# Optimization experiments

Hardware: AMD Instinct MI355X
Metric: run time of the kernel (lower is better)

Reference implementation:

```python
import jax, jax.numpy as jnp
from jax import lax
import numpy as np

GROUPS = 32  # EMA 'factor'
EPS = 1e-5   # torch GroupNorm default eps


def setup_inputs() -> dict:
    key = jax.random.key(0)
    ks = jax.random.split(key, 3)
    B, C, H, W = 8, 256, 128, 128
    cg = C // GROUPS  # channels per group = 8
    x = jax.random.normal(ks[0], (B, C, H, W), dtype=jnp.float32)
    w1 = jax.random.normal(ks[1], (cg, cg), dtype=jnp.float32) * 0.1    # conv1x1 weight (O,I)
    b1 = jnp.zeros((cg,), dtype=jnp.float32)
    w3 = jax.random.normal(ks[2], (cg, cg, 3, 3), dtype=jnp.float32) * 0.1  # conv3x3 weight (O,I,kh,kw)
    b3 = jnp.zeros((cg,), dtype=jnp.float32)
    gn_w = jnp.ones((cg,), dtype=jnp.float32)
    gn_b = jnp.zeros((cg,), dtype=jnp.float32)
    return {"x": x, "w1": w1, "b1": b1, "w3": w3, "b3": b3, "gn_w": gn_w, "gn_b": gn_b}


def reference(x, w1, b1, w3, b3, gn_w, gn_b):
    b, c, h, w = x.shape
    g = GROUPS
    cg = c // g
    gx = x.reshape(b * g, cg, h, w)                       # [bg, cg, h, w]
    # directional pooling (AdaptiveAvgPool over one axis)
    x_h = gx.mean(axis=3, keepdims=True)                  # [bg, cg, h, 1]
    x_w = gx.mean(axis=2, keepdims=True).transpose(0, 1, 3, 2)  # [bg, cg, w, 1]
    hw = jnp.concatenate([x_h, x_w], axis=2)              # [bg, cg, h+w, 1]
    hw = jnp.einsum('oi,bilk->bolk', w1, hw) + b1[None, :, None, None]
    xh = hw[:, :, :h]                                      # [bg, cg, h, 1]
    xw = hw[:, :, h:].transpose(0, 1, 3, 2)                # [bg, cg, 1, w]
    gated = gx * jax.nn.sigmoid(xh) * jax.nn.sigmoid(xw)
    # GroupNorm(cg groups over cg channels) == per-channel norm over (h, w)
    mu = gated.mean(axis=(2, 3), keepdims=True)
    var = gated.var(axis=(2, 3), keepdims=True)
    x1 = (gated - mu) / jnp.sqrt(var + EPS) * gn_w[None, :, None, None] + gn_b[None, :, None, None]
    # 3x3 conv branch
    x2 = lax.conv_general_dilated(gx, w3, (1, 1), 'SAME',
                                  dimension_numbers=('NCHW', 'OIHW', 'NCHW'))
    x2 = x2 + b3[None, :, None, None]
    # cross-branch channel-attention matmuls
    x11 = jax.nn.softmax(x1.mean(axis=(2, 3)), axis=-1)[:, None, :]  # [bg, 1, cg]
    x21 = jax.nn.softmax(x2.mean(axis=(2, 3)), axis=-1)[:, None, :]  # [bg, 1, cg]
    x12 = x2.reshape(b * g, cg, h * w)
    x22 = x1.reshape(b * g, cg, h * w)
    weights = (jnp.matmul(x11, x12) + jnp.matmul(x21, x22)).reshape(b * g, 1, h, w)
    return (gx * jax.nn.sigmoid(weights)).reshape(b, c, h, w)
```

## Files before the change

### kernel.cpp

```cpp
#include <hip/hip_runtime.h>
#include <cstdint>

#define EPS 1e-5f
#define TS 136

__global__ __launch_bounds__(1024) void k1_gates(
    const float* __restrict__ x,
    const float* __restrict__ w1, const float* __restrict__ b1,
    const float* __restrict__ w3, const float* __restrict__ b3,
    const float* __restrict__ gn_b,
    float* __restrict__ sh, float* __restrict__ sw,
    float* __restrict__ x21, float* __restrict__ wt)
{
    __shared__ float rs[1024], cs[1024];
    __shared__ float4 red[1024];
    __shared__ float w1l[64], b1l[8], corn[32], S[8], Tm[72], m2[8], x11[8];
    const int bg = blockIdx.x;
    const int t  = threadIdx.x;
    const int sg = t >> 8, ts = t & 255;
    const size_t pbase = (size_t)(bg * 8) * 16384;

    for (int half = 0; half < 2; ++half) {
        int pi = half * 4 + sg;
        const float4* xp = (const float4*)(x + pbase + (size_t)pi * 16384);
        float4 csum = {0.f, 0.f, 0.f, 0.f};
        for (int i = 0; i < 16; ++i) {
            float4 v = xp[i * 256 + ts];
            csum.x += v.x; csum.y += v.y; csum.z += v.z; csum.w += v.w;
            float rsv = v.x + v.y + v.z + v.w;
            for (int m = 16; m; m >>= 1) rsv += __shfl_xor(rsv, m);
            if ((ts & 31) == 0) rs[pi * 128 + i * 8 + (ts >> 5)] = rsv;
        }
        red[sg * 256 + ts] = csum;
        __syncthreads();
        if (ts < 32) {
            float4 s = red[sg * 256 + ts];
            for (int j = 1; j < 8; ++j) {
                float4 v = red[sg * 256 + j * 32 + ts];
                s.x += v.x; s.y += v.y; s.z += v.z; s.w += v.w;
            }
            ((float4*)(cs + pi * 128))[ts] = s;
        }
        __syncthreads();
    }

    if (t < 64) w1l[t] = w1[t];
    if (t >= 64 && t < 72) b1l[t - 64] = b1[t - 64];
    if (t >= 128 && t < 136) {
        int i = t - 128;
        const float* xpp = x + pbase + (size_t)i * 16384;
        corn[i * 4 + 0] = xpp[0];
        corn[i * 4 + 1] = xpp[127];
        corn[i * 4 + 2] = xpp[127 * 128];
        corn[i * 4 + 3] = xpp[127 * 128 + 127];
    }
    if (t == 200) {
        float mx = gn_b[0];
        for (int i = 1; i < 8; ++i) mx = fmaxf(mx, gn_b[i]);
        float e[8], s = 0.f;
        for (int i = 0; i < 8; ++i) { e[i] = __expf(gn_b[i] - mx); s += e[i]; }
        for (int i = 0; i < 8; ++i) x11[i] = e[i] / s;
    }
    __syncthreads();

    {
        int o = t >> 7, y = t & 127;
        const float inv128 = 1.f / 128.f;
        float ar = b1l[o], ac = ar;
        for (int i = 0; i < 8; ++i) {
            float w = w1l[o * 8 + i];
            ar += w * rs[i * 128 + y] * inv128;
            ac += w * cs[i * 128 + y] * inv128;
        }
        sh[(bg * 8 + o) * 128 + y] = 1.f / (1.f + __expf(-ar));
        sw[(bg * 8 + o) * 128 + y] = 1.f / (1.f + __expf(-ac));
    }
    if (t < 8) {
        float s = 0.f;
        for (int y = 0; y < 128; ++y) s += rs[t * 128 + y];
        S[t] = s;
    }
    __syncthreads();

    if (t < 72) {
        int i = t / 9, ky = (t % 9) / 3, kx = t % 3;
        float v = S[i];
        if (ky == 0) v -= rs[i * 128 + 127]; else if (ky == 2) v -= rs[i * 128 + 0];
        if (kx == 0) v -= cs[i * 128 + 127]; else if (kx == 2) v -= cs[i * 128 + 0];
        if (ky == 0 && kx == 0) v += corn[i * 4 + 3];
        if (ky == 0 && kx == 2) v += corn[i * 4 + 2];
        if (ky == 2 && kx == 0) v += corn[i * 4 + 1];
        if (ky == 2 && kx == 2) v += corn[i * 4 + 0];
        Tm[t] = v;
    }
    __syncthreads();

    if (t < 8) {
        float acc = 0.f;
        for (int j = 0; j < 72; ++j) acc += w3[t * 72 + j] * Tm[j];
        m2[t] = b3[t] + acc * (1.f / 16384.f);
    }
    if (bg == 0 && t >= 128 && t < 201) {
        int j = t - 128;
        float a = 0.f;
        if (j < 72) { for (int o = 0; o < 8; ++o) a += x11[o] * w3[o * 72 + j]; }
        else        { for (int o = 0; o < 8; ++o) a += x11[o] * b3[o]; }
        wt[j] = a;
    }
    __syncthreads();

    if (t == 0) {
        float mx = m2[0];
        for (int i = 1; i < 8; ++i) mx = fmaxf(mx, m2[i]);
        float e[8], s = 0.f;
        for (int i = 0; i < 8; ++i) { e[i] = __expf(m2[i] - mx); s += e[i]; }
        for (int i = 0; i < 8; ++i) x21[bg * 8 + i] = e[i] / s;
    }
}

__global__ __launch_bounds__(1024) void k2_stats(
    const float* __restrict__ x, const float* __restrict__ sh,
    const float* __restrict__ sw, const float* __restrict__ x21,
    const float* __restrict__ gn_w, const float* __restrict__ gn_b,
    const float* __restrict__ wt,
    float* __restrict__ alpha, float* __restrict__ beta)
{
    __shared__ float shl[1024], swl[1024], ps[64], qs[64], bs[8];
    const int bg = blockIdx.x;
    const int t  = threadIdx.x;
    const int sg = t >> 8, ts = t & 255;
    const size_t pbase = (size_t)(bg * 8) * 16384;
    shl[t] = sh[bg * 1024 + t];
    swl[t] = sw[bg * 1024 + t];
    __syncthreads();

    for (int half = 0; half < 2; ++half) {
        int pi = half * 4 + sg;
        const float4* xp = (const float4*)(x + pbase + (size_t)pi * 16384);
        float4 sw4 = ((const float4*)(swl + pi * 128))[ts & 31];
        float s = 0.f, q = 0.f;
        for (int i = 0; i < 16; ++i) {
            float4 v = xp[i * 256 + ts];
            float shv = shl[pi * 128 + i * 8 + (ts >> 5)];
            float g0 = v.x * shv * sw4.x;
            float g1 = v.y * shv * sw4.y;
            float g2 = v.z * shv * sw4.z;
            float g3 = v.w * shv * sw4.w;
            s += g0 + g1 + g2 + g3;
            q += g0 * g0 + g1 * g1 + g2 * g2 + g3 * g3;
        }
        for (int m = 16; m; m >>= 1) { s += __shfl_xor(s, m); q += __shfl_xor(q, m); }
        if ((ts & 31) == 0) {
            ps[pi * 8 + (ts >> 5)] = s;
            qs[pi * 8 + (ts >> 5)] = q;
        }
    }
    __syncthreads();
    if (t < 8) {
        float s = 0.f, q = 0.f;
        for (int j = 0; j < 8; ++j) { s += ps[t * 8 + j]; q += qs[t * 8 + j]; }
        float mu  = s * (1.f / 16384.f);
        float ex2 = q * (1.f / 16384.f);
        float var = ex2 - mu * mu;
        float inv = rsqrtf(var + EPS);
        float x21v = x21[bg * 8 + t];
        alpha[bg * 8 + t] = x21v * inv * gn_w[t];
        bs[t] = x21v * (gn_b[t] - mu * inv * gn_w[t]);
    }
    __syncthreads();
    if (t == 0) {
        float s = wt[72];
        for (int i = 0; i < 8; ++i) s += bs[i];
        beta[bg] = s;
    }
}

__global__ __launch_bounds__(256, 2) void k3_out(
    const float* __restrict__ x, const float* __restrict__ sh,
    const float* __restrict__ sw, const float* __restrict__ alpha,
    const float* __restrict__ beta, const float* __restrict__ wt,
    float* __restrict__ out)
{
    __shared__ float tl[8 * 18 * TS];
    __shared__ float wtl[73], al[8];
    __shared__ float betal;
    const int blk = blockIdx.x;
    const int bg  = blk >> 3;
    const int r0  = (blk & 7) * 16;
    const int t    = threadIdx.x;
    const int lane = t & 31;
    const int cidx = t >> 5;
    const size_t pbase = (size_t)(bg * 8) * 16384;

    {
        const float* xc = x + pbase + (size_t)cidx * 16384 + 4 * lane;
        float* dst = tl + (cidx * 18) * TS + 4 + 4 * lane;
#pragma unroll
        for (int row = 0; row < 18; ++row) {
            int g = r0 - 1 + row;
            float4 v = {0.f, 0.f, 0.f, 0.f};
            if ((unsigned)g < 128u) v = *(const float4*)(xc + (size_t)g * 128);
            *(float4*)(dst + row * TS) = v;
        }
        if (lane == 0 || lane == 31) {
            float* pz = tl + (cidx * 18) * TS + (lane == 0 ? 0 : 132);
            float4 z = {0.f, 0.f, 0.f, 0.f};
#pragma unroll
            for (int row = 0; row < 18; ++row) *(float4*)(pz + row * TS) = z;
        }
    }
    if (t < 73) wtl[t] = wt[t];
    else if (t < 81) al[t - 73] = alpha[bg * 8 + (t - 73)];
    else if (t == 81) betal = beta[bg];
    __syncthreads();

    const int yg = cidx;
    const int y0 = r0 + 2 * yg;
    const int x0 = 4 * lane;
    float4 accA = {betal, betal, betal, betal};
    float4 accB = accA;
    float4 gvA[8], gvB[8];

#pragma unroll
    for (int i = 0; i < 8; ++i) {
        const float* B = tl + (i * 18 + 2 * yg) * TS + 4 + x0;
        float asA = al[i] * sh[(size_t)(bg * 8 + i) * 128 + y0];
        float asB = al[i] * sh[(size_t)(bg * 8 + i) * 128 + y0 + 1];
        float4 s4 = *(const float4*)(sw + (size_t)(bg * 8 + i) * 128 + x0);
#pragma unroll
        for (int r = 0; r < 4; ++r) {
            float4 v = *(const float4*)(B + r * TS);
            float xm1 = __shfl_up(v.w, 1, 32);
            if (lane == 0)  xm1 = 0.f;
            float xp4 = __shfl_down(v.x, 1, 32);
            if (lane == 31) xp4 = 0.f;
            if (r < 3) {
                float w0 = wtl[i * 9 + r * 3 + 0];
                float w1v = wtl[i * 9 + r * 3 + 1];
                float w2 = wtl[i * 9 + r * 3 + 2];
                accA.x += w0 * xm1  + w1v * v.x + w2 * v.y;
                accA.y += w0 * v.x  + w1v * v.y + w2 * v.z;
                accA.z += w0 * v.y  + w1v * v.z + w2 * v.w;
                accA.w += w0 * v.z  + w1v * v.w + w2 * xp4;
            }
            if (r > 0) {
                int ky = r - 1;
                float w0 = wtl[i * 9 + ky * 3 + 0];
                float w1v = wtl[i * 9 + ky * 3 + 1];
                float w2 = wtl[i * 9 + ky * 3 + 2];
                accB.x += w0 * xm1  + w1v * v.x + w2 * v.y;
                accB.y += w0 * v.x  + w1v * v.y + w2 * v.z;
                accB.z += w0 * v.y  + w1v * v.z + w2 * v.w;
                accB.w += w0 * v.z  + w1v * v.w + w2 * xp4;
            }
            if (r == 1) gvA[i] = v;
            if (r == 2) gvB[i] = v;
        }
        accA.x += asA * s4.x * gvA[i].x;
        accA.y += asA * s4.y * gvA[i].y;
        accA.z += asA * s4.z * gvA[i].z;
        accA.w += asA * s4.w * gvA[i].w;
        accB.x += asB * s4.x * gvB[i].x;
        accB.y += asB * s4.y * gvB[i].y;
        accB.z += asB * s4.z * gvB[i].z;
        accB.w += asB * s4.w * gvB[i].w;
    }

    float4 sgA, sgB;
    sgA.x = 1.f / (1.f + __expf(-accA.x));
    sgA.y = 1.f / (1.f + __expf(-accA.y));
    sgA.z = 1.f / (1.f + __expf(-accA.z));
    sgA.w = 1.f / (1.f + __expf(-accA.w));
    sgB.x = 1.f / (1.f + __expf(-accB.x));
    sgB.y = 1.f / (1.f + __expf(-accB.y));
    sgB.z = 1.f / (1.f + __expf(-accB.z));
    sgB.w = 1.f / (1.f + __expf(-accB.w));

    size_t ob = pbase + (size_t)y0 * 128 + x0;
#pragma unroll
    for (int c = 0; c < 8; ++c) {
        float4 oA = { gvA[c].x * sgA.x, gvA[c].y * sgA.y, gvA[c].z * sgA.z, gvA[c].w * sgA.w };
        float4 oB = { gvB[c].x * sgB.x, gvB[c].y * sgB.y, gvB[c].z * sgB.z, gvB[c].w * sgB.w };
        *(float4*)(out + ob + (size_t)c * 16384)       = oA;
        *(float4*)(out + ob + (size_t)c * 16384 + 128) = oB;
    }
}

extern "C" void kernel_launch(void* const* d_in, const int* in_sizes, int n_in,
                              void* d_out, int out_size, void* d_ws, size_t ws_size,
                              hipStream_t stream) {
    (void)in_sizes; (void)n_in; (void)out_size; (void)ws_size;
    const float* x    = (const float*)d_in[0];
    const float* w1   = (const float*)d_in[1];
    const float* b1   = (const float*)d_in[2];
    const float* w3   = (const float*)d_in[3];
    const float* b3   = (const float*)d_in[4];
    const float* gn_w = (const float*)d_in[5];
    const float* gn_b = (const float*)d_in[6];
    float* out = (float*)d_out;
    float* ws  = (float*)d_ws;

    float* sh    = ws;
    float* sw    = ws + 262144;
    float* x21   = ws + 524288;
    float* alpha = ws + 526336;
    float* beta  = ws + 528384;
    float* wt    = ws + 528640;

    hipLaunchKernelGGL(k1_gates, dim3(256),  dim3(1024), 0, stream,
                       x, w1, b1, w3, b3, gn_b, sh, sw, x21, wt);
    hipLaunchKernelGGL(k2_stats, dim3(256),  dim3(1024), 0, stream,
                       x, sh, sw, x21, gn_w, gn_b, wt, alpha, beta);
    hipLaunchKernelGGL(k3_out,   dim3(2048), dim3(256),  0, stream,
                       x, sh, sw, alpha, beta, wt, out);
}
```

Before: 107.6 us.

## Split pooling sums into wide kernel, merge gate and stats, drop LDS tile

```diff
diff --git a/kernel.cpp b/kernel.cpp
--- a/kernel.cpp
+++ b/kernel.cpp
@@ -2,48 +2,54 @@
 #include <cstdint>
 
 #define EPS 1e-5f
-#define TS 136
-
-__global__ __launch_bounds__(1024) void k1_gates(
+
+__global__ __launch_bounds__(256) void k1_sums(const float* __restrict__ x,
+                                               float* __restrict__ rowsum,
+                                               float* __restrict__ colsum) {
+    int p = blockIdx.x;
+    int t = threadIdx.x;
+    const float4* xp = (const float4*)(x + (size_t)p * 16384);
+    float4 csum = {0.f, 0.f, 0.f, 0.f};
+    for (int i = 0; i < 16; ++i) {
+        float4 v = xp[i * 256 + t];
+        csum.x += v.x; csum.y += v.y; csum.z += v.z; csum.w += v.w;
+        float rs = v.x + v.y + v.z + v.w;
+        for (int m = 16; m; m >>= 1) rs += __shfl_xor(rs, m);
+        if ((t & 31) == 0) rowsum[p * 128 + i * 8 + (t >> 5)] = rs;
+    }
+    __shared__ float4 red[256];
+    red[t] = csum;
+    __syncthreads();
+    if (t < 32) {
+        float4 s = red[t];
+        for (int j = 1; j < 8; ++j) {
+            float4 v = red[j * 32 + t];
+            s.x += v.x; s.y += v.y; s.z += v.z; s.w += v.w;
+        }
+        ((float4*)colsum)[p * 32 + t] = s;
+    }
+}
+
+__global__ __launch_bounds__(1024) void k2_mid(
     const float* __restrict__ x,
+    const float* __restrict__ rowsum, const float* __restrict__ colsum,
     const float* __restrict__ w1, const float* __restrict__ b1,
     const float* __restrict__ w3, const float* __restrict__ b3,
-    const float* __restrict__ gn_b,
+    const float* __restrict__ gn_w, const float* __restrict__ gn_b,
     float* __restrict__ sh, float* __restrict__ sw,
-    float* __restrict__ x21, float* __restrict__ wt)
+    float* __restrict__ wt, float* __restrict__ alpha, float* __restrict__ beta)
 {
-    __shared__ float rs[1024], cs[1024];
-    __shared__ float4 red[1024];
-    __shared__ float w1l[64], b1l[8], corn[32], S[8], Tm[72], m2[8], x11[8];
+    __shared__ float rs[1024], cs[1024], shl[1024], swl[1024];
+    __shared__ float w1l[64], b1l[8], corn[32], S[8], Tm[72], m2[8], x11[8], x21l[8];
+    __shared__ float ps[64], qs[64], bs[8];
+    __shared__ float btl;
     const int bg = blockIdx.x;
     const int t  = threadIdx.x;
     const int sg = t >> 8, ts = t & 255;
     const size_t pbase = (size_t)(bg * 8) * 16384;
 
-    for (int half = 0; half < 2; ++half) {
-        int pi = half * 4 + sg;
-        const float4* xp = (const float4*)(x + pbase + (size_t)pi * 16384);
-        float4 csum = {0.f, 0.f, 0.f, 0.f};
-        for (int i = 0; i < 16; ++i) {
-            float4 v = xp[i * 256 + ts];
-            csum.x += v.x; csum.y += v.y; csum.z += v.z; csum.w += v.w;
-            float rsv = v.x + v.y + v.z + v.w;
-            for (int m = 16; m; m >>= 1) rsv += __shfl_xor(rsv, m);
-            if ((ts & 31) == 0) rs[pi * 128 + i * 8 + (ts >> 5)] = rsv;
-        }
-        red[sg * 256 + ts] = csum;
-        __syncthreads();
-        if (ts < 32) {
-            float4 s = red[sg * 256 + ts];
-            for (int j = 1; j < 8; ++j) {
-                float4 v = red[sg * 256 + j * 32 + ts];
-                s.x += v.x; s.y += v.y; s.z += v.z; s.w += v.w;
-            }
-            ((float4*)(cs + pi * 128))[ts] = s;
-        }
-        __syncthreads();
-    }
-
+    rs[t] = rowsum[bg * 1024 + t];
+    cs[t] = colsum[bg * 1024 + t];
     if (t < 64) w1l[t] = w1[t];
     if (t >= 64 && t < 72) b1l[t - 64] = b1[t - 64];
     if (t >= 128 && t < 136) {
@@ -63,6 +69,11 @@
     }
     __syncthreads();
 
+    if (t == 300) {
+        float a = 0.f;
+        for (int o = 0; o < 8; ++o) a += x11[o] * b3[o];
+        btl = a;
+    }
     {
         int o = t >> 7, y = t & 127;
         const float inv128 = 1.f / 128.f;
@@ -72,8 +83,10 @@
             ar += w * rs[i * 128 + y] * inv128;
             ac += w * cs[i * 128 + y] * inv128;
         }
-        sh[(bg * 8 + o) * 128 + y] = 1.f / (1.f + __expf(-ar));
-        sw[(bg * 8 + o) * 128 + y] = 1.f / (1.f + __expf(-ac));
+        float sv = 1.f / (1.f + __expf(-ar));
+        float wv = 1.f / (1.f + __expf(-ac));
+        shl[o * 128 + y] = sv;  sh[(bg * 8 + o) * 128 + y] = sv;
+        swl[o * 128 + y] = wv;  sw[(bg * 8 + o) * 128 + y] = wv;
     }
     if (t < 8) {
         float s = 0.f;
@@ -100,11 +113,10 @@
         for (int j = 0; j < 72; ++j) acc += w3[t * 72 + j] * Tm[j];
         m2[t] = b3[t] + acc * (1.f / 16384.f);
     }
-    if (bg == 0 && t >= 128 && t < 201) {
+    if (bg == 0 && t >= 128 && t < 200) {
         int j = t - 128;
         float a = 0.f;
-        if (j < 72) { for (int o = 0; o < 8; ++o) a += x11[o] * w3[o * 72 + j]; }
-        else        { for (int o = 0; o < 8; ++o) a += x11[o] * b3[o]; }
+        for (int o = 0; o < 8; ++o) a += x11[o] * w3[o * 72 + j];
         wt[j] = a;
     }
     __syncthreads();
@@ -114,24 +126,8 @@
         for (int i = 1; i < 8; ++i) mx = fmaxf(mx, m2[i]);
         float e[8], s = 0.f;
         for (int i = 0; i < 8; ++i) { e[i] = __expf(m2[i] - mx); s += e[i]; }
-        for (int i = 0; i < 8; ++i) x21[bg * 8 + i] = e[i] / s;
-    }
-}
-
-__global__ __launch_bounds__(1024) void k2_stats(
-    const float* __restrict__ x, const float* __restrict__ sh,
-    const float* __restrict__ sw, const float* __restrict__ x21,
-    const float* __restrict__ gn_w, const float* __restrict__ gn_b,
-    const float* __restrict__ wt,
-    float* __restrict__ alpha, float* __restrict__ beta)
-{
-    __shared__ float shl[1024], swl[1024], ps[64], qs[64], bs[8];
-    const int bg = blockIdx.x;
-    const int t  = threadIdx.x;
-    const int sg = t >> 8, ts = t & 255;
-    const size_t pbase = (size_t)(bg * 8) * 16384;
-    shl[t] = sh[bg * 1024 + t];
-    swl[t] = sw[bg * 1024 + t];
+        for (int i = 0; i < 8; ++i) x21l[i] = e[i] / s;
+    }
     __syncthreads();
 
     for (int half = 0; half < 2; ++half) {
@@ -163,107 +159,103 @@
         float ex2 = q * (1.f / 16384.f);
         float var = ex2 - mu * mu;
         float inv = rsqrtf(var + EPS);
-        float x21v = x21[bg * 8 + t];
+        float x21v = x21l[t];
         alpha[bg * 8 + t] = x21v * inv * gn_w[t];
         bs[t] = x21v * (gn_b[t] - mu * inv * gn_w[t]);
     }
     __syncthreads();
     if (t == 0) {
-        float s = wt[72];
+        float s = btl;
         for (int i = 0; i < 8; ++i) s += bs[i];
         beta[bg] = s;
     }
 }
 
-__global__ __launch_bounds__(256, 2) void k3_out(
+__global__ __launch_bounds__(256) void k3_out(
     const float* __restrict__ x, const float* __restrict__ sh,
     const float* __restrict__ sw, const float* __restrict__ alpha,
     const float* __restrict__ beta, const float* __restrict__ wt,
     float* __restrict__ out)
 {
-    __shared__ float tl[8 * 18 * TS];
-    __shared__ float wtl[73], al[8];
+    __shared__ float wtl[72], al[8], shl[128], swl[1024];
     __shared__ float betal;
-    const int blk = blockIdx.x;
-    const int bg  = blk >> 3;
-    const int r0  = (blk & 7) * 16;
-    const int t    = threadIdx.x;
-    const int lane = t & 31;
-    const int cidx = t >> 5;
+    const int blk = blockIdx.x, bg = blk >> 3, r0 = (blk & 7) * 16;
+    const int t = threadIdx.x, lane = t & 31, yg = t >> 5;
     const size_t pbase = (size_t)(bg * 8) * 16384;
 
-    {
-        const float* xc = x + pbase + (size_t)cidx * 16384 + 4 * lane;
-        float* dst = tl + (cidx * 18) * TS + 4 + 4 * lane;
-#pragma unroll
-        for (int row = 0; row < 18; ++row) {
-            int g = r0 - 1 + row;
-            float4 v = {0.f, 0.f, 0.f, 0.f};
-            if ((unsigned)g < 128u) v = *(const float4*)(xc + (size_t)g * 128);
-            *(float4*)(dst + row * TS) = v;
-        }
-        if (lane == 0 || lane == 31) {
-            float* pz = tl + (cidx * 18) * TS + (lane == 0 ? 0 : 132);
-            float4 z = {0.f, 0.f, 0.f, 0.f};
-#pragma unroll
-            for (int row = 0; row < 18; ++row) *(float4*)(pz + row * TS) = z;
-        }
-    }
-    if (t < 73) wtl[t] = wt[t];
-    else if (t < 81) al[t - 73] = alpha[bg * 8 + (t - 73)];
-    else if (t == 81) betal = beta[bg];
-    __syncthreads();
-
-    const int yg = cidx;
+    if (t < 72) wtl[t] = wt[t];
+    if (t >= 72 && t < 80) al[t - 72] = alpha[bg * 8 + (t - 72)];
+    if (t == 80) betal = beta[bg];
+    if (t >= 96 && t < 224) {
+        int j = t - 96;
+        shl[j] = sh[(size_t)(bg * 8 + (j >> 4)) * 128 + r0 + (j & 15)];
+    }
+    ((float4*)swl)[t] = ((const float4*)sw)[(size_t)(bg * 8 + yg) * 32 + lane];
+    __syncthreads();
+
     const int y0 = r0 + 2 * yg;
-    const int x0 = 4 * lane;
+    const int x0 = lane * 4;
     float4 accA = {betal, betal, betal, betal};
     float4 accB = accA;
-    float4 gvA[8], gvB[8];
+    const float4 z4 = {0.f, 0.f, 0.f, 0.f};
 
 #pragma unroll
     for (int i = 0; i < 8; ++i) {
-        const float* B = tl + (i * 18 + 2 * yg) * TS + 4 + x0;
-        float asA = al[i] * sh[(size_t)(bg * 8 + i) * 128 + y0];
-        float asB = al[i] * sh[(size_t)(bg * 8 + i) * 128 + y0 + 1];
-        float4 s4 = *(const float4*)(sw + (size_t)(bg * 8 + i) * 128 + x0);
-#pragma unroll
-        for (int r = 0; r < 4; ++r) {
-            float4 v = *(const float4*)(B + r * TS);
-            float xm1 = __shfl_up(v.w, 1, 32);
-            if (lane == 0)  xm1 = 0.f;
-            float xp4 = __shfl_down(v.x, 1, 32);
-            if (lane == 31) xp4 = 0.f;
-            if (r < 3) {
-                float w0 = wtl[i * 9 + r * 3 + 0];
-                float w1v = wtl[i * 9 + r * 3 + 1];
-                float w2 = wtl[i * 9 + r * 3 + 2];
-                accA.x += w0 * xm1  + w1v * v.x + w2 * v.y;
-                accA.y += w0 * v.x  + w1v * v.y + w2 * v.z;
-                accA.z += w0 * v.y  + w1v * v.z + w2 * v.w;
-                accA.w += w0 * v.z  + w1v * v.w + w2 * xp4;
-            }
-            if (r > 0) {
-                int ky = r - 1;
-                float w0 = wtl[i * 9 + ky * 3 + 0];
-                float w1v = wtl[i * 9 + ky * 3 + 1];
-                float w2 = wtl[i * 9 + ky * 3 + 2];
-                accB.x += w0 * xm1  + w1v * v.x + w2 * v.y;
-                accB.y += w0 * v.x  + w1v * v.y + w2 * v.z;
-                accB.z += w0 * v.y  + w1v * v.z + w2 * v.w;
-                accB.w += w0 * v.z  + w1v * v.w + w2 * xp4;
-            }
-            if (r == 1) gvA[i] = v;
-            if (r == 2) gvB[i] = v;
-        }
-        accA.x += asA * s4.x * gvA[i].x;
-        accA.y += asA * s4.y * gvA[i].y;
-        accA.z += asA * s4.z * gvA[i].z;
-        accA.w += asA * s4.w * gvA[i].w;
-        accB.x += asB * s4.x * gvB[i].x;
-        accB.y += asB * s4.y * gvB[i].y;
-        accB.z += asB * s4.z * gvB[i].z;
-        accB.w += asB * s4.w * gvB[i].w;
+        const float* bp = x + pbase + (size_t)i * 16384 + x0;
+        float4 v0 = (y0 - 1 >= 0)  ? *(const float4*)(bp + (y0 - 1) * 128) : z4;
+        float4 v1 = *(const float4*)(bp + y0 * 128);
+        float4 v2 = *(const float4*)(bp + (y0 + 1) * 128);
+        float4 v3 = (y0 + 2 < 128) ? *(const float4*)(bp + (y0 + 2) * 128) : z4;
+
+        float m0 = __shfl_up(v0.w, 1, 32); if (lane == 0) m0 = 0.f;
+        float m1 = __shfl_up(v1.w, 1, 32); if (lane == 0) m1 = 0.f;
+        float m2v = __shfl_up(v2.w, 1, 32); if (lane == 0) m2v = 0.f;
+        float m3 = __shfl_up(v3.w, 1, 32); if (lane == 0) m3 = 0.f;
+        float p0 = __shfl_down(v0.x, 1, 32); if (lane == 31) p0 = 0.f;
+        float p1 = __shfl_down(v1.x, 1, 32); if (lane == 31) p1 = 0.f;
+        float p2 = __shfl_down(v2.x, 1, 32); if (lane == 31) p2 = 0.f;
+        float p3 = __shfl_down(v3.x, 1, 32); if (lane == 31) p3 = 0.f;
+
+        float w00 = wtl[i * 9 + 0], w01 = wtl[i * 9 + 1], w02 = wtl[i * 9 + 2];
+        float w10 = wtl[i * 9 + 3], w11 = wtl[i * 9 + 4], w12 = wtl[i * 9 + 5];
+        float w20 = wtl[i * 9 + 6], w21 = wtl[i * 9 + 7], w22 = wtl[i * 9 + 8];
+
+        accA.x += w00 * m0   + w01 * v0.x + w02 * v0.y;
+        accA.y += w00 * v0.x + w01 * v0.y + w02 * v0.z;
+        accA.z += w00 * v0.y + w01 * v0.z + w02 * v0.w;
+        accA.w += w00 * v0.z + w01 * v0.w + w02 * p0;
+        accA.x += w10 * m1   + w11 * v1.x + w12 * v1.y;
+        accA.y += w10 * v1.x + w11 * v1.y + w12 * v1.z;
+        accA.z += w10 * v1.y + w11 * v1.z + w12 * v1.w;
+        accA.w += w10 * v1.z + w11 * v1.w + w12 * p1;
+        accA.x += w20 * m2v  + w21 * v2.x + w22 * v2.y;
+        accA.y += w20 * v2.x + w21 * v2.y + w22 * v2.z;
+        accA.z += w20 * v2.y + w21 * v2.z + w22 * v2.w;
+        accA.w += w20 * v2.z + w21 * v2.w + w22 * p2;
+        accB.x += w00 * m1   + w01 * v1.x + w02 * v1.y;
+        accB.y += w00 * v1.x + w01 * v1.y + w02 * v1.z;
+        accB.z += w00 * v1.y + w01 * v1.z + w02 * v1.w;
+        accB.w += w00 * v1.z + w01 * v1.w + w02 * p1;
+        accB.x += w10 * m2v  + w11 * v2.x + w12 * v2.y;
+        accB.y += w10 * v2.x + w11 * v2.y + w12 * v2.z;
+        accB.z += w10 * v2.y + w11 * v2.z + w12 * v2.w;
+        accB.w += w10 * v2.z + w11 * v2.w + w12 * p2;
+        accB.x += w20 * m3   + w21 * v3.x + w22 * v3.y;
+        accB.y += w20 * v3.x + w21 * v3.y + w22 * v3.z;
+        accB.z += w20 * v3.y + w21 * v3.z + w22 * v3.w;
+        accB.w += w20 * v3.z + w21 * v3.w + w22 * p3;
+
+        float asA = al[i] * shl[i * 16 + 2 * yg];
+        float asB = al[i] * shl[i * 16 + 2 * yg + 1];
+        float4 s4 = *(const float4*)(swl + i * 128 + x0);
+        accA.x += asA * s4.x * v1.x;
+        accA.y += asA * s4.y * v1.y;
+        accA.z += asA * s4.z * v1.z;
+        accA.w += asA * s4.w * v1.w;
+        accB.x += asB * s4.x * v2.x;
+        accB.y += asB * s4.y * v2.y;
+        accB.z += asB * s4.z * v2.z;
+        accB.w += asB * s4.w * v2.w;
     }
 
     float4 sgA, sgB;
@@ -279,8 +271,11 @@
     size_t ob = pbase + (size_t)y0 * 128 + x0;
 #pragma unroll
     for (int c = 0; c < 8; ++c) {
-        float4 oA = { gvA[c].x * sgA.x, gvA[c].y * sgA.y, gvA[c].z * sgA.z, gvA[c].w * sgA.w };
-        float4 oB = { gvB[c].x * sgB.x, gvB[c].y * sgB.y, gvB[c].z * sgB.z, gvB[c].w * sgB.w };
+        const float* bp = x + pbase + (size_t)c * 16384 + x0;
+        float4 c1 = *(const float4*)(bp + y0 * 128);
+        float4 c2 = *(const float4*)(bp + (y0 + 1) * 128);
+        float4 oA = { c1.x * sgA.x, c1.y * sgA.y, c1.z * sgA.z, c1.w * sgA.w };
+        float4 oB = { c2.x * sgB.x, c2.y * sgB.y, c2.z * sgB.z, c2.w * sgB.w };
         *(float4*)(out + ob + (size_t)c * 16384)       = oA;
         *(float4*)(out + ob + (size_t)c * 16384 + 128) = oB;
     }
@@ -300,17 +295,17 @@
     float* out = (float*)d_out;
     float* ws  = (float*)d_ws;
 
-    float* sh    = ws;
-    float* sw    = ws + 262144;
-    float* x21   = ws + 524288;
-    float* alpha = ws + 526336;
-    float* beta  = ws + 528384;
-    float* wt    = ws + 528640;
-
-    hipLaunchKernelGGL(k1_gates, dim3(256),  dim3(1024), 0, stream,
-                       x, w1, b1, w3, b3, gn_b, sh, sw, x21, wt);
-    hipLaunchKernelGGL(k2_stats, dim3(256),  dim3(1024), 0, stream,
-                       x, sh, sw, x21, gn_w, gn_b, wt, alpha, beta);
-    hipLaunchKernelGGL(k3_out,   dim3(2048), dim3(256),  0, stream,
-                       x, sh, sw, alpha, beta, wt, out);
+    float* rowsum = ws;
+    float* colsum = ws + 262144;
+    float* sh     = ws + 524288;
+    float* sw     = ws + 786432;
+    float* alpha  = ws + 1048576;
+    float* beta   = ws + 1050624;
+    float* wt     = ws + 1050880;
+
+    hipLaunchKernelGGL(k1_sums, dim3(2048), dim3(256),  0, stream, x, rowsum, colsum);
+    hipLaunchKernelGGL(k2_mid,  dim3(256),  dim3(1024), 0, stream, x, rowsum, colsum,
+                       w1, b1, w3, b3, gn_w, gn_b, sh, sw, wt, alpha, beta);
+    hipLaunchKernelGGL(k3_out,  dim3(2048), dim3(256),  0, stream, x, sh, sw,
+                       alpha, beta, wt, out);
 }
```

Measured after the change: 147.7 us. 1.37x slower.
